# Performance work log

Hardware: AMD Instinct MI355X
Metric: run time of the kernel (lower is better)

## Reference

```python
import jax, jax.numpy as jnp
import numpy as np

# q_config constants
W_IN, E_IN = 8, 4          # data_in_width, data_in_exponent_width
R_W = 6                     # data_r_width
W_OUT, E_OUT = 8, 4        # data_out_width, data_out_exponent_width (= data_n_width)
EXP_SUM_UF = 4              # exp_sum_underflow_bits
DIV_UF = 4                  # division_underflow_bits
W_DATA, E_DATA = 8, 4      # data_width, data_exponent_width

N, D = 8192, 2048


def integer_quantizer(x, width, frac_width):
    s = 2.0 ** frac_width
    lo, hi = -(2.0 ** (width - 1)), 2.0 ** (width - 1) - 1
    return jnp.clip(jnp.round(x * s), lo, hi) / s


def integer_floor_quantizer(x, width, frac_width):
    s = 2.0 ** frac_width
    lo, hi = -(2.0 ** (width - 1)), 2.0 ** (width - 1) - 1
    return jnp.clip(jnp.floor(x * s), lo, hi) / s


def mxint_quant(x, width, exponent_width):
    # MXInt block quantization with parallelism [1,1]: per-element shared exponent.
    e_hi, e_lo = 2.0 ** (exponent_width - 1) - 1, -(2.0 ** (exponent_width - 1))
    ax = jnp.abs(x)
    e = jnp.ceil(jnp.log2(jnp.where(ax == 0, 1.0, ax)))
    e = jnp.clip(e, e_lo, e_hi)
    scale = 2.0 ** (width - 1)
    m = jnp.clip(jnp.round(x * 2.0 ** (-e) * scale), -scale, scale - 1)
    qx = m * 2.0 ** e / scale
    return qx, m, e


def setup_inputs() -> dict:
    key = jax.random.key(0)
    x = jax.random.normal(key, (N, D), dtype=jnp.float32)
    return {"x": x}


def reference(x):
    # ---- MXIntHardwareExp: quantize input, range-reduce x = r + n*ln2 ----
    qx, _, _ = mxint_quant(x, W_IN, E_IN)
    log2e, _, _ = mxint_quant(jnp.float32(np.log2(np.e)), 8, 4)
    y = qx * log2e
    y = integer_floor_quantizer(y, E_OUT + R_W - 1, R_W - 1)
    n = jnp.floor(y)
    r = y - n                                # r in [0, 1)
    mexp = integer_quantizer(2.0 ** r, W_OUT, W_OUT - 2) * 2.0 ** (W_OUT - 2)
    eexp = n                                 # qexp = mexp * 2^eexp / 2^(W_OUT-2)

    # ---- exp_sum: exponent-aligned integer accumulation over dim 1 ----
    ms = (mexp * 2.0 ** EXP_SUM_UF).T        # [D, N]
    es = eexp.T                              # [D, N]

    def step(carry, me):
        out, emax = carry
        mi, ei = me
        new_emax = jnp.maximum(emax, ei)
        out = jnp.floor(out * 2.0 ** (emax - new_emax)) + jnp.floor(mi * 2.0 ** (ei - new_emax))
        return (out, new_emax), None

    (mexp_sum, eexp_sum), _ = jax.lax.scan(step, (ms[0], es[0]), (ms[1:], es[1:]))
    # mexp_sum, eexp_sum: [N]

    # ---- division: per-element mantissa integer division by the sum ----
    mout = jnp.floor(mexp * 2.0 ** (DIV_UF + EXP_SUM_UF) / mexp_sum[:, None])
    eout = eexp - eexp_sum[:, None]
    qout = mout * 2.0 ** eout / 2.0 ** DIV_UF
    qout, _, _ = mxint_quant(qout, W_DATA, E_DATA)
    return qout
```

## Files before the change

### kernel.cpp

```cpp
#include <hip/hip_runtime.h>


#define D_DIM 2048
#define TPB   256

__device__ __forceinline__ unsigned bmax4(unsigned x, unsigned y) {
    const unsigned d     = (x | 0x80808080u) - y;
    const unsigned flags = d & 0x80808080u;
    const unsigned mask  = (flags - (flags >> 7)) | flags;
    return (x & mask) | (y & ~mask);
}

__global__ __launch_bounds__(TPB, 6) void mxint_softmax_kernel(const float* __restrict__ x,
                                                               float* __restrict__ out) {
    const int t    = threadIdx.x;
    const int lane = t & 63;
    const int wid  = t >> 6;
    const int half = wid & 1;
    const int r    = wid >> 1;
    const int row  = blockIdx.x * 2 + r;

    __shared__ unsigned short     s_pk[512];
    __shared__ float              s_fin[2][512];
    __shared__ int                s_rmax[4];
    __shared__ unsigned long long s_part[4];

    const size_t base = (size_t)row * D_DIM + half * 1024 + lane * 4;
    float4 v[4];
#pragma unroll
    for (int i = 0; i < 4; ++i)
        v[i] = *(const float4*)(x + base + i * 256);

#pragma unroll
    for (int q = 0; q < 2; ++q) {
        const int idx = t + 256 * q;
        const float a = fmaf((float)(idx & 31), 0.03125f, 6.0f);
        const int  me = (int)rintf(__builtin_amdgcn_exp2f(a));
        s_pk[idx] = (unsigned short)(me << 4);
    }

    int yq[16];
    unsigned pe = 0;
#pragma unroll
    for (int i = 0; i < 4; ++i) {
        const float xs4[4] = {v[i].x, v[i].y, v[i].z, v[i].w};
        int rmaxr = -256;
#pragma unroll
        for (int k = 0; k < 4; ++k) {
            const unsigned b  = __float_as_uint(xs4[k]) & 0x7fffffffu;
            const unsigned tb = b + 0x7fffffu;
            const unsigned tc = min(max(tb, 0x3B800000u), 0x43000000u);
            const unsigned es = tc & 0xFF800000u;
            const float    su  = __uint_as_float(0x82800000u - es);
            const float    fac = __uint_as_float(es + 0xFF380000u);
            const float    mi  = __builtin_amdgcn_fmed3f(rintf(xs4[k] * su), -128.0f, 127.0f);
            int y = (int)floorf(mi * fac);
            y = min(255, max(-256, y));
            yq[4 * i + k] = y;
            rmaxr = max(rmaxr, y);
        }
        pe |= (unsigned)((rmaxr >> 5) + 8) << (8 * i);
    }

    unsigned s = pe;
#pragma unroll
    for (int d = 1; d < 64; d <<= 1) {
        const unsigned o = __shfl_up(s, d, 64);
        if (lane >= d) s = bmax4(s, o);
    }
    unsigned ex = __shfl_up(s, 1, 64);
    if (lane == 0) ex = 0;
    const unsigned bc = __shfl(s, 63, 64);
    const int wtot = max(max((int)(bc & 255u), (int)((bc >> 8) & 255u)),
                         max((int)((bc >> 16) & 255u), (int)(bc >> 24)));
    s_rmax[wid] = wtot;
    __syncthreads();

    const int c0 = half ? s_rmax[wid - 1] : 0;

    unsigned partial = 0;
    int crun = c0;
#pragma unroll
    for (int i = 0; i < 4; ++i) {
        const int sx   = (int)((ex >> (8 * i)) & 255u);
        int a = max(crun, sx);
#pragma unroll
        for (int k = 0; k < 4; ++k) {
            const int y  = yq[4 * i + k];
            const int h  = (y >> 5) + 8;
            a = max(a, h);
            const unsigned me4 = s_pk[y + 256];
            partial += (me4 >> (a - h)) << a;
        }
        crun = max(crun, (int)((bc >> (8 * i)) & 255u));
    }

    const unsigned ps = partial + __shfl_xor(partial, 1, 64);
    unsigned long long p64 = ps;
#pragma unroll
    for (int d = 2; d < 64; d <<= 1) p64 += __shfl_xor(p64, d, 64);
    s_part[wid] = p64;
    __syncthreads();

    const unsigned long long tot = s_part[2 * r] + s_part[2 * r + 1];
    const int      Estar8 = max(s_rmax[2 * r], s_rmax[2 * r + 1]);
    const unsigned msum   = (unsigned)(tot >> Estar8);
    const unsigned magic  = (unsigned)(274877906944.0 / (double)msum) + 1u;

    const int tr = t & 127;
#pragma unroll
    for (int q = 0; q < 4; ++q) {
        const int      idx  = tr + 128 * q;
        const unsigned me4  = s_pk[idx];
        const unsigned mout = __umulhi(me4 << 4, magic) >> 6;
        const int      e8   = idx >> 5;
        const int      eoutn = Estar8 - e8;
        const int      bl   = 32 - __clz((int)(mout | 1u));
        const int      pw2  = ((mout & (mout - 1u)) == 0u) ? 1 : 0;
        const int      clog = bl - pw2;
        const int      sq   = min(7 - clog, 11 - eoutn);
        const int      rs   = 8 - sq;
        const unsigned u    = mout << 8;
        const unsigned bse  = u >> rs;
        const unsigned frac = u & ((1u << rs) - 1u);
        const unsigned hlf  = 1u << (rs - 1);
        unsigned m2 = bse + (((frac > hlf) || (frac == hlf && (bse & 1u))) ? 1u : 0u);
        m2 = min(m2, 127u);
        const int ef = max(clog - eoutn - 4, -8);
        s_fin[r][idx] = (float)m2 * __uint_as_float((unsigned)(ef + 120) << 23);
    }
    __syncthreads();

    float* orow = out + base;
#pragma unroll
    for (int i = 0; i < 4; ++i) {
        float r4[4];
#pragma unroll
        for (int k = 0; k < 4; ++k)
            r4[k] = s_fin[r][yq[4 * i + k] + 256];
        const float4 o4 = {r4[0], r4[1], r4[2], r4[3]};
        *(float4*)(orow + i * 256) = o4;
    }
}

extern "C" void kernel_launch(void* const* d_in, const int* in_sizes, int n_in,
                              void* d_out, int out_size, void* d_ws, size_t ws_size,
                              hipStream_t stream) {
    const float* x = (const float*)d_in[0];
    float*       o = (float*)d_out;
    const int rows = in_sizes[0] / D_DIM;
    mxint_softmax_kernel<<<rows / 2, TPB, 0, stream>>>(x, o);
}
```

Before: 109.7 us.

## Use one row per 128-thread block with per-wave output table, drop final barrier

Each block now handles a single row with two waves instead of two rows with four waves, doubling the grid. Each wave builds its own copy of the 512-entry output lookup table so the final __syncthreads can be dropped. The y index is biased by 256 using an FMA so the table lookups need no offset. The cost is duplicated table computation per wave and more, smaller blocks. The launch_bounds occupancy hint of 6 is unchanged while the block size halves.

```diff
diff --git a/kernel.cpp b/kernel.cpp
--- a/kernel.cpp
+++ b/kernel.cpp
@@ -2,7 +2,7 @@
 
 
 #define D_DIM 2048
-#define TPB   256
+#define TPB   128
 
 __device__ __forceinline__ unsigned bmax4(unsigned x, unsigned y) {
     const unsigned d     = (x | 0x80808080u) - y;
@@ -16,35 +16,32 @@
     const int t    = threadIdx.x;
     const int lane = t & 63;
     const int wid  = t >> 6;
-    const int half = wid & 1;
-    const int r    = wid >> 1;
-    const int row  = blockIdx.x * 2 + r;
 
     __shared__ unsigned short     s_pk[512];
     __shared__ float              s_fin[2][512];
-    __shared__ int                s_rmax[4];
-    __shared__ unsigned long long s_part[4];
+    __shared__ int                s_rmax[2];
+    __shared__ unsigned long long s_part[2];
 
-    const size_t base = (size_t)row * D_DIM + half * 1024 + lane * 4;
+    const size_t base = (size_t)blockIdx.x * D_DIM + wid * 1024 + lane * 4;
     float4 v[4];
 #pragma unroll
     for (int i = 0; i < 4; ++i)
         v[i] = *(const float4*)(x + base + i * 256);
 
 #pragma unroll
-    for (int q = 0; q < 2; ++q) {
-        const int idx = t + 256 * q;
+    for (int q = 0; q < 4; ++q) {
+        const int idx = t + TPB * q;
         const float a = fmaf((float)(idx & 31), 0.03125f, 6.0f);
         const int  me = (int)rintf(__builtin_amdgcn_exp2f(a));
         s_pk[idx] = (unsigned short)(me << 4);
     }
 
-    int yq[16];
+    int yb[16];
     unsigned pe = 0;
 #pragma unroll
     for (int i = 0; i < 4; ++i) {
         const float xs4[4] = {v[i].x, v[i].y, v[i].z, v[i].w};
-        int rmaxr = -256;
+        int rmax = 0;
 #pragma unroll
         for (int k = 0; k < 4; ++k) {
             const unsigned b  = __float_as_uint(xs4[k]) & 0x7fffffffu;
@@ -54,12 +51,12 @@
             const float    su  = __uint_as_float(0x82800000u - es);
             const float    fac = __uint_as_float(es + 0xFF380000u);
             const float    mi  = __builtin_amdgcn_fmed3f(rintf(xs4[k] * su), -128.0f, 127.0f);
-            int y = (int)floorf(mi * fac);
-            y = min(255, max(-256, y));
-            yq[4 * i + k] = y;
-            rmaxr = max(rmaxr, y);
+            int y = (int)fmaf(mi, fac, 256.0f);
+            y = min(511, max(0, y));
+            yb[4 * i + k] = y;
+            rmax = max(rmax, y);
         }
-        pe |= (unsigned)((rmaxr >> 5) + 8) << (8 * i);
+        pe |= (unsigned)(rmax >> 5) << (8 * i);
     }
 
     unsigned s = pe;
@@ -73,23 +70,23 @@
     const unsigned bc = __shfl(s, 63, 64);
     const int wtot = max(max((int)(bc & 255u), (int)((bc >> 8) & 255u)),
                          max((int)((bc >> 16) & 255u), (int)(bc >> 24)));
-    s_rmax[wid] = wtot;
+    if (lane == 0) s_rmax[wid] = wtot;
     __syncthreads();
 
-    const int c0 = half ? s_rmax[wid - 1] : 0;
+    const int c0 = wid ? s_rmax[0] : 0;
 
     unsigned partial = 0;
     int crun = c0;
 #pragma unroll
     for (int i = 0; i < 4; ++i) {
-        const int sx   = (int)((ex >> (8 * i)) & 255u);
+        const int sx = (int)((ex >> (8 * i)) & 255u);
         int a = max(crun, sx);
 #pragma unroll
         for (int k = 0; k < 4; ++k) {
-            const int y  = yq[4 * i + k];
-            const int h  = (y >> 5) + 8;
+            const int y = yb[4 * i + k];
+            const int h = y >> 5;
             a = max(a, h);
-            const unsigned me4 = s_pk[y + 256];
+            const unsigned me4 = s_pk[y];
             partial += (me4 >> (a - h)) << a;
         }
         crun = max(crun, (int)((bc >> (8 * i)) & 255u));
@@ -99,37 +96,35 @@
     unsigned long long p64 = ps;
 #pragma unroll
     for (int d = 2; d < 64; d <<= 1) p64 += __shfl_xor(p64, d, 64);
-    s_part[wid] = p64;
+    if (lane == 0) s_part[wid] = p64;
     __syncthreads();
 
-    const unsigned long long tot = s_part[2 * r] + s_part[2 * r + 1];
-    const int      Estar8 = max(s_rmax[2 * r], s_rmax[2 * r + 1]);
+    const unsigned long long tot = s_part[0] + s_part[1];
+    const int      Estar8 = max(s_rmax[0], s_rmax[1]);
     const unsigned msum   = (unsigned)(tot >> Estar8);
     const unsigned magic  = (unsigned)(274877906944.0 / (double)msum) + 1u;
 
-    const int tr = t & 127;
+    float* fin = s_fin[wid];
 #pragma unroll
-    for (int q = 0; q < 4; ++q) {
-        const int      idx  = tr + 128 * q;
-        const unsigned me4  = s_pk[idx];
-        const unsigned mout = __umulhi(me4 << 4, magic) >> 6;
-        const int      e8   = idx >> 5;
-        const int      eoutn = Estar8 - e8;
-        const int      bl   = 32 - __clz((int)(mout | 1u));
-        const int      pw2  = ((mout & (mout - 1u)) == 0u) ? 1 : 0;
-        const int      clog = bl - pw2;
-        const int      sq   = min(7 - clog, 11 - eoutn);
-        const int      rs   = 8 - sq;
-        const unsigned u    = mout << 8;
-        const unsigned bse  = u >> rs;
-        const unsigned frac = u & ((1u << rs) - 1u);
-        const unsigned hlf  = 1u << (rs - 1);
+    for (int q = 0; q < 8; ++q) {
+        const int      idx   = lane + 64 * q;
+        const unsigned me4   = s_pk[idx];
+        const unsigned mout  = __umulhi((unsigned)me4 << 4, magic) >> 6;
+        const int      eoutn = Estar8 - (idx >> 5);
+        const int      bl    = 32 - __clz((int)(mout | 1u));
+        const int      pw2   = ((mout & (mout - 1u)) == 0u) ? 1 : 0;
+        const int      clog  = bl - pw2;
+        const int      sq    = min(7 - clog, 11 - eoutn);
+        const int      rs    = 8 - sq;
+        const unsigned u     = mout << 8;
+        const unsigned bse   = u >> rs;
+        const unsigned frac  = u & ((1u << rs) - 1u);
+        const unsigned hlf   = 1u << (rs - 1);
         unsigned m2 = bse + (((frac > hlf) || (frac == hlf && (bse & 1u))) ? 1u : 0u);
         m2 = min(m2, 127u);
         const int ef = max(clog - eoutn - 4, -8);
-        s_fin[r][idx] = (float)m2 * __uint_as_float((unsigned)(ef + 120) << 23);
+        fin[idx] = (float)m2 * __uint_as_float((unsigned)(ef + 120) << 23);
     }
-    __syncthreads();
 
     float* orow = out + base;
 #pragma unroll
@@ -137,7 +132,7 @@
         float r4[4];
 #pragma unroll
         for (int k = 0; k < 4; ++k)
-            r4[k] = s_fin[r][yq[4 * i + k] + 256];
+            r4[k] = fin[yb[4 * i + k]];
         const float4 o4 = {r4[0], r4[1], r4[2], r4[3]};
         *(float4*)(orow + i * 256) = o4;
     }
@@ -149,5 +144,5 @@
     const float* x = (const float*)d_in[0];
     float*       o = (float*)d_out;
     const int rows = in_sizes[0] / D_DIM;
-    mxint_softmax_kernel<<<rows / 2, TPB, 0, stream>>>(x, o);
+    mxint_softmax_kernel<<<rows, TPB, 0, stream>>>(x, o);
 }
```

Result: no change. 110.8 us (+1.0%).
